# Kernel optimization log

Hardware: AMD Instinct MI355X
Metric: run time of the kernel (lower is better)

Reference implementation:

```python
import jax, jax.numpy as jnp
import numpy as np

HEAD_DIM = 64
SCALE = 1.0 / np.sqrt(HEAD_DIM).astype(np.float32)
EPS = 1e-6


def setup_inputs() -> dict:
    key = jax.random.key(0)
    kq, kk, kv = jax.random.split(key, 3)
    shape = (2, 16, 2048, HEAD_DIM)  # [B, H, S, D]
    return {
        "q": jax.random.normal(kq, shape, dtype=jnp.float32),
        "k": jax.random.normal(kk, shape, dtype=jnp.float32),
        "v": jax.random.normal(kv, shape, dtype=jnp.float32),
    }


def reference(q, k, v):
    # scores: [B, H, S, S]
    scores = jnp.einsum("bhqd,bhkd->bhqk", q, k) * SCALE
    num = scores * scores  # p = 2 power normalization
    den = num.sum(axis=-1, keepdims=True) + EPS
    prob = num / den
    out = jnp.einsum("bhqk,bhkd->bhqd", prob, v)
    return (out, prob)
```

## Files before the change

### kernel.cpp

```cpp
#include <hip/hip_runtime.h>
#include <stdint.h>

#define S_LEN 2048
#define D_DIM 64
#define NBH   32
#define TQ    128
#define KT    64
#define NT    (S_LEN / KT)
#define RC_G  8
#define SCALE_F 0.125f
#define EPS_F   1e-6f
#define SPSTR 40

typedef unsigned short us;
typedef __attribute__((ext_vector_type(8))) short bf8_t;
typedef __attribute__((ext_vector_type(4))) float f4_t;
typedef __attribute__((ext_vector_type(16))) float f16_t;
typedef __attribute__((ext_vector_type(4))) unsigned int u4_t;

#define MFMA16(a,b,c) __builtin_amdgcn_mfma_f32_16x16x32_bf16((a),(b),(c),0,0,0)
#define MFMA32(a,b,c) __builtin_amdgcn_mfma_f32_32x32x16_bf16((a),(b),(c),0,0,0)

__device__ __forceinline__ unsigned int cvtpk(float lo, float hi) {
  unsigned int d;
  asm("v_cvt_pk_bf16_f32 %0, %1, %2" : "=v"(d) : "v"(lo), "v"(hi));
  return d;
}

union u4bf8 { u4_t u; bf8_t b; };

__global__ __launch_bounds__(256) void g_kernel(const float* __restrict__ kp,
                                                float* __restrict__ gpart) {
  __shared__ __align__(16) float sk[64][68];
  const int bh = blockIdx.x >> 3, rc = blockIdx.x & 7;
  const int t = threadIdx.x;
  const int ti = t >> 4, tj = t & 15;
  float acc[4][4];
#pragma unroll
  for (int a = 0; a < 4; ++a)
#pragma unroll
    for (int b = 0; b < 4; ++b) acc[a][b] = 0.f;
  const float* kb = kp + ((size_t)bh * S_LEN + rc * 256) * D_DIM;
  for (int sub = 0; sub < 4; ++sub) {
    __syncthreads();
    {
      const int r = t >> 2, c0 = (t & 3) * 16;
      const float4* p = (const float4*)(kb + (size_t)(sub * 64 + r) * D_DIM + c0);
      float4 x0 = p[0], x1 = p[1], x2 = p[2], x3 = p[3];
      *(float4*)&sk[r][c0]      = x0;
      *(float4*)&sk[r][c0 + 4]  = x1;
      *(float4*)&sk[r][c0 + 8]  = x2;
      *(float4*)&sk[r][c0 + 12] = x3;
    }
    __syncthreads();
#pragma unroll 4
    for (int r = 0; r < 64; ++r) {
      float4 qi = *(const float4*)&sk[r][ti * 4];
      float4 qj = *(const float4*)&sk[r][tj * 4];
      float iv[4] = {qi.x, qi.y, qi.z, qi.w};
      float jv[4] = {qj.x, qj.y, qj.z, qj.w};
#pragma unroll
      for (int a = 0; a < 4; ++a)
#pragma unroll
        for (int b = 0; b < 4; ++b) acc[a][b] += iv[a] * jv[b];
    }
  }
  float* gb = gpart + ((size_t)(rc * NBH + bh) << 12);
#pragma unroll
  for (int a = 0; a < 4; ++a) {
    f4_t vv = {acc[a][0], acc[a][1], acc[a][2], acc[a][3]};
    *(f4_t*)(gb + (ti * 4 + a) * 64 + tj * 4) = vv;
  }
}

__device__ __forceinline__ bf8_t frag_swz(const us* sp, int row, int cb) {
  return *(const bf8_t*)(sp + row * 64 + ((cb ^ (row & 7)) << 3));
}

__global__ __launch_bounds__(512, 4) void attn_main(const float* __restrict__ q,
                                                    const float* __restrict__ k,
                                                    const float* __restrict__ v,
                                                    const float* __restrict__ gpart,
                                                    float* __restrict__ outp,
                                                    float* __restrict__ probp) {
  __shared__ __align__(16) unsigned char smem[53248];
  us* sK  = (us*)smem;
  us* sVt = (us*)(smem + 16384);
  us* sP  = (us*)(smem + 32768);
  float* sInv = (float*)(smem + 32768);
  float* sRed = (float*)smem;

  const int lin = blockIdx.x;
  const int virt = (lin & 7) * 64 + (lin >> 3);
  const int bh = virt >> 4, qb = virt & 15;
  const int q0 = qb * TQ;
  const int t = threadIdx.x, lane = t & 63, w = t >> 6;
  const int l31 = lane & 31, hi = lane >> 5;
  const int wq = w & 3, kh = w >> 2;

  const float* kbh = k + (size_t)bh * S_LEN * D_DIM;
  const float* vbh = v + (size_t)bh * S_LEN * D_DIM;
  const float* qbh = q + (size_t)bh * S_LEN * D_DIM;

  const int kr = t >> 3, kc = t & 7;
  const int vr = (t & 31) * 2, vc = (t >> 5) * 4;

  float4 pk0, pk1, pva, pvb;
  {
    const float4* kp_ = (const float4*)(kbh + (size_t)kr * D_DIM + kc * 8);
    pk0 = kp_[0]; pk1 = kp_[1];
    const float4* vp0 = (const float4*)(vbh + (size_t)vr * D_DIM + vc);
    const float4* vp1 = (const float4*)(vbh + (size_t)(vr + 1) * D_DIM + vc);
    pva = vp0[0]; pvb = vp1[0];
  }

  bf8_t qA[4];
  {
    const float* qrow = qbh + (size_t)(q0 + wq * 32 + l31) * D_DIM;
#pragma unroll
    for (int s = 0; s < 4; ++s) {
      const float4* qp = (const float4*)(qrow + s * 16 + hi * 8);
      float4 a = qp[0], b = qp[1];
      u4bf8 x;
      x.u[0] = cvtpk(a.x * SCALE_F, a.y * SCALE_F);
      x.u[1] = cvtpk(a.z * SCALE_F, a.w * SCALE_F);
      x.u[2] = cvtpk(b.x * SCALE_F, b.y * SCALE_F);
      x.u[3] = cvtpk(b.z * SCALE_F, b.w * SCALE_F);
      qA[s] = x.b;
    }
  }

  {
    const float* gp = gpart + ((size_t)bh << 12) + (size_t)kr * D_DIM + kc * 8;
    const size_t gstride = (size_t)NBH << 12;
    float4 a = {0.f, 0.f, 0.f, 0.f}, b = {0.f, 0.f, 0.f, 0.f};
#pragma unroll
    for (int rc = 0; rc < RC_G; ++rc) {
      const float4* p = (const float4*)(gp + rc * gstride);
      float4 x = p[0], y = p[1];
      a.x += x.x; a.y += x.y; a.z += x.z; a.w += x.w;
      b.x += y.x; b.y += y.y; b.z += y.z; b.w += y.w;
    }
    u4bf8 x;
    x.u[0] = cvtpk(a.x, a.y); x.u[1] = cvtpk(a.z, a.w);
    x.u[2] = cvtpk(b.x, b.y); x.u[3] = cvtpk(b.z, b.w);
    *(u4_t*)(sK + kr * 64 + ((kc ^ (kr & 7)) << 3)) = x.u;
  }
  __syncthreads();

  {
    const int lr = lane & 15, lh = lane >> 4;
    bf8_t qD[2];
    {
      const float* qbase = qbh + (size_t)(q0 + w * 16 + lr) * D_DIM;
#pragma unroll
      for (int h2 = 0; h2 < 2; ++h2) {
        const float4* qp = (const float4*)(qbase + h2 * 32 + lh * 8);
        float4 a = qp[0], b = qp[1];
        u4bf8 x;
        x.u[0] = cvtpk(a.x * SCALE_F, a.y * SCALE_F);
        x.u[1] = cvtpk(a.z * SCALE_F, a.w * SCALE_F);
        x.u[2] = cvtpk(b.x * SCALE_F, b.y * SCALE_F);
        x.u[3] = cvtpk(b.z * SCALE_F, b.w * SCALE_F);
        qD[h2] = x.b;
      }
    }
    float den[4] = {0.f, 0.f, 0.f, 0.f};
#pragma unroll
    for (int ct = 0; ct < 4; ++ct) {
      f4_t accT = {0.f, 0.f, 0.f, 0.f};
      bf8_t b0 = frag_swz(sK, ct * 16 + lr, lh);
      bf8_t b1 = frag_swz(sK, ct * 16 + lr, 4 + lh);
      accT = MFMA16(qD[0], b0, accT);
      accT = MFMA16(qD[1], b1, accT);
#pragma unroll
      for (int i = 0; i < 4; ++i) {
        float qv = qbh[(size_t)(q0 + w * 16 + lh * 4 + i) * D_DIM + ct * 16 + lr] * SCALE_F;
        den[i] += accT[i] * qv;
      }
    }
#pragma unroll
    for (int i = 0; i < 4; ++i) {
      den[i] += __shfl_xor(den[i], 1, 64);
      den[i] += __shfl_xor(den[i], 2, 64);
      den[i] += __shfl_xor(den[i], 4, 64);
      den[i] += __shfl_xor(den[i], 8, 64);
      sInv[w * 16 + lh * 4 + i] = 1.f / (den[i] + EPS_F);
    }
  }
  __syncthreads();

  float invv[16];
#pragma unroll
  for (int r = 0; r < 16; ++r)
    invv[r] = sInv[wq * 32 + (r & 3) + 8 * (r >> 2) + 4 * hi];
  __syncthreads();

  {
    u4bf8 x;
    x.u[0] = cvtpk(pk0.x, pk0.y); x.u[1] = cvtpk(pk0.z, pk0.w);
    x.u[2] = cvtpk(pk1.x, pk1.y); x.u[3] = cvtpk(pk1.z, pk1.w);
    *(u4_t*)(sK + kr * 64 + ((kc ^ (kr & 7)) << 3)) = x.u;
    unsigned int w0 = cvtpk(pva.x, pvb.x), w1 = cvtpk(pva.y, pvb.y);
    unsigned int w2 = cvtpk(pva.z, pvb.z), w3 = cvtpk(pva.w, pvb.w);
    const int cks = vr >> 3, sub = vr & 7;
    *(unsigned int*)(sVt + (vc + 0) * 64 + ((cks ^ ((vc + 0) & 7)) << 3) + sub) = w0;
    *(unsigned int*)(sVt + (vc + 1) * 64 + ((cks ^ ((vc + 1) & 7)) << 3) + sub) = w1;
    *(unsigned int*)(sVt + (vc + 2) * 64 + ((cks ^ ((vc + 2) & 7)) << 3) + sub) = w2;
    *(unsigned int*)(sVt + (vc + 3) * 64 + ((cks ^ ((vc + 3) & 7)) << 3) + sub) = w3;
  }
  __syncthreads();

  f16_t oaccA, oaccB;
#pragma unroll
  for (int i = 0; i < 16; ++i) { oaccA[i] = 0.f; oaccB[i] = 0.f; }

  us* sPw = sP + w * (32 * SPSTR);
  float* probw = probp + ((size_t)bh * S_LEN + q0 + wq * 32) * S_LEN + kh * 32 + l31;

  for (int kt = 0; kt < NT; ++kt) {
    const int cur = kt & 1, nxt = cur ^ 1;
    const us* sKc = sK + cur * 4096;
    const us* sVc = sVt + cur * 4096;
    us* sKn = sK + nxt * 4096;
    us* sVn = sVt + nxt * 4096;
    const int k0 = kt * KT;

    if (kt + 1 < NT) {
      const int k0n = k0 + KT;
      const float4* kp_ = (const float4*)(kbh + (size_t)(k0n + kr) * D_DIM + kc * 8);
      pk0 = kp_[0]; pk1 = kp_[1];
      const float4* vp0 = (const float4*)(vbh + (size_t)(k0n + vr) * D_DIM + vc);
      const float4* vp1 = (const float4*)(vbh + (size_t)(k0n + vr + 1) * D_DIM + vc);
      pva = vp0[0]; pvb = vp1[0];
    }

    f16_t cacc;
#pragma unroll
    for (int i = 0; i < 16; ++i) cacc[i] = 0.f;
#pragma unroll
    for (int s = 0; s < 4; ++s) {
      bf8_t bk = frag_swz(sKc, kh * 32 + l31, 2 * s + hi);
      cacc = MFMA32(qA[s], bk, cacc);
    }

#pragma unroll
    for (int a = 0; a < 4; ++a) {
      float p0 = cacc[4 * a + 0] * cacc[4 * a + 0] * invv[4 * a + 0];
      float p1 = cacc[4 * a + 1] * cacc[4 * a + 1] * invv[4 * a + 1];
      float p2 = cacc[4 * a + 2] * cacc[4 * a + 2] * invv[4 * a + 2];
      float p3 = cacc[4 * a + 3] * cacc[4 * a + 3] * invv[4 * a + 3];
      const int qq = 8 * a + 4 * hi;
      __builtin_nontemporal_store(p0, probw + (size_t)(qq + 0) * S_LEN + k0);
      __builtin_nontemporal_store(p1, probw + (size_t)(qq + 1) * S_LEN + k0);
      __builtin_nontemporal_store(p2, probw + (size_t)(qq + 2) * S_LEN + k0);
      __builtin_nontemporal_store(p3, probw + (size_t)(qq + 3) * S_LEN + k0);
      unsigned int c01 = cvtpk(p0, p1);
      unsigned int c23 = cvtpk(p2, p3);
      sPw[(qq + 0) * SPSTR + l31] = (us)(c01 & 0xffffu);
      sPw[(qq + 1) * SPSTR + l31] = (us)(c01 >> 16);
      sPw[(qq + 2) * SPSTR + l31] = (us)(c23 & 0xffffu);
      sPw[(qq + 3) * SPSTR + l31] = (us)(c23 >> 16);
    }

    bf8_t pa0 = *(const bf8_t*)(sPw + l31 * SPSTR + 0 * 16 + hi * 8);
    bf8_t pa1 = *(const bf8_t*)(sPw + l31 * SPSTR + 1 * 16 + hi * 8);

    bf8_t vb00 = frag_swz(sVc, 0 * 32 + l31, kh * 4 + 2 * 0 + hi);
    bf8_t vb01 = frag_swz(sVc, 1 * 32 + l31, kh * 4 + 2 * 0 + hi);
    bf8_t vb10 = frag_swz(sVc, 0 * 32 + l31, kh * 4 + 2 * 1 + hi);
    bf8_t vb11 = frag_swz(sVc, 1 * 32 + l31, kh * 4 + 2 * 1 + hi);

    oaccA = MFMA32(pa0, vb00, oaccA);
    oaccB = MFMA32(pa0, vb01, oaccB);
    oaccA = MFMA32(pa1, vb10, oaccA);
    oaccB = MFMA32(pa1, vb11, oaccB);

    if (kt + 1 < NT) {
      u4bf8 x;
      x.u[0] = cvtpk(pk0.x, pk0.y); x.u[1] = cvtpk(pk0.z, pk0.w);
      x.u[2] = cvtpk(pk1.x, pk1.y); x.u[3] = cvtpk(pk1.z, pk1.w);
      *(u4_t*)(sKn + kr * 64 + ((kc ^ (kr & 7)) << 3)) = x.u;
      unsigned int w0 = cvtpk(pva.x, pvb.x), w1 = cvtpk(pva.y, pvb.y);
      unsigned int w2 = cvtpk(pva.z, pvb.z), w3 = cvtpk(pva.w, pvb.w);
      const int cks = vr >> 3, sub = vr & 7;
      *(unsigned int*)(sVn + (vc + 0) * 64 + ((cks ^ ((vc + 0) & 7)) << 3) + sub) = w0;
      *(unsigned int*)(sVn + (vc + 1) * 64 + ((cks ^ ((vc + 1) & 7)) << 3) + sub) = w1;
      *(unsigned int*)(sVn + (vc + 2) * 64 + ((cks ^ ((vc + 2) & 7)) << 3) + sub) = w2;
      *(unsigned int*)(sVn + (vc + 3) * 64 + ((cks ^ ((vc + 3) & 7)) << 3) + sub) = w3;
    }
    __syncthreads();
  }

  if (kh == 1) {
    float* dst = sRed + wq * 2048;
#pragma unroll
    for (int i = 0; i < 4; ++i) {
      f4_t ga = {oaccA[4 * i], oaccA[4 * i + 1], oaccA[4 * i + 2], oaccA[4 * i + 3]};
      f4_t gb = {oaccB[4 * i], oaccB[4 * i + 1], oaccB[4 * i + 2], oaccB[4 * i + 3]};
      *(f4_t*)(dst + 0 * 1024 + i * 256 + lane * 4) = ga;
      *(f4_t*)(dst + 1 * 1024 + i * 256 + lane * 4) = gb;
    }
  }
  __syncthreads();
  if (kh == 0) {
    const float* src = sRed + wq * 2048;
    float* ob = outp + ((size_t)bh * S_LEN + q0 + wq * 32) * D_DIM + l31;
#pragma unroll
    for (int i = 0; i < 4; ++i) {
      f4_t ga = *(const f4_t*)(src + 0 * 1024 + i * 256 + lane * 4);
      f4_t gb = *(const f4_t*)(src + 1 * 1024 + i * 256 + lane * 4);
#pragma unroll
      for (int b = 0; b < 4; ++b) {
        const int r = 4 * i + b;
        const int qr = (r & 3) + 8 * (r >> 2) + 4 * hi;
        __builtin_nontemporal_store(oaccA[r] + ga[b], ob + (size_t)qr * D_DIM + 0);
        __builtin_nontemporal_store(oaccB[r] + gb[b], ob + (size_t)qr * D_DIM + 32);
      }
    }
  }
}

extern "C" void kernel_launch(void* const* d_in, const int* in_sizes, int n_in,
                              void* d_out, int out_size, void* d_ws, size_t ws_size,
                              hipStream_t stream) {
  (void)in_sizes; (void)n_in; (void)out_size; (void)ws_size;
  const float* q = (const float*)d_in[0];
  const float* k = (const float*)d_in[1];
  const float* v = (const float*)d_in[2];
  float* outp  = (float*)d_out;
  float* probp = outp + (size_t)NBH * S_LEN * D_DIM;
  float* gpart = (float*)d_ws;

  g_kernel<<<dim3(NBH * RC_G), dim3(256), 0, stream>>>(k, gpart);
  attn_main<<<dim3(512), dim3(512), 0, stream>>>(q, k, v, gpart, outp, probp);
}
```

Baseline: 139.0 us.

## Stage prob tiles in swizzled LDS and write them back as float4 rows

The bf16 P tile for two key tiles is kept in a larger, XOR-swizzled LDS buffer shared by the whole block. Every second iteration, the block reads it back and writes 128-column row segments of prob to global memory with vectorized nontemporal float4 stores. This replaces the per-lane scalar stores and aims for wider, better-coalesced writes of the prob output, which dominates memory traffic. The cost is extra LDS use (64 KB), which may lower occupancy, plus an extra barrier. Prob values are now written from bf16-rounded data, so the output loses precision compared with the fp32 values it stored before.

```diff
diff --git a/kernel.cpp b/kernel.cpp
--- a/kernel.cpp
+++ b/kernel.cpp
@@ -10,7 +10,6 @@
 #define RC_G  8
 #define SCALE_F 0.125f
 #define EPS_F   1e-6f
-#define SPSTR 40
 
 typedef unsigned short us;
 typedef __attribute__((ext_vector_type(8))) short bf8_t;
@@ -83,10 +82,10 @@
                                                     const float* __restrict__ gpart,
                                                     float* __restrict__ outp,
                                                     float* __restrict__ probp) {
-  __shared__ __align__(16) unsigned char smem[53248];
+  __shared__ __align__(16) unsigned char smem[65536];
   us* sK  = (us*)smem;
   us* sVt = (us*)(smem + 16384);
-  us* sP  = (us*)(smem + 32768);
+  unsigned char* Pb = smem + 32768;
   float* sInv = (float*)(smem + 32768);
   float* sRed = (float*)smem;
 
@@ -215,9 +214,6 @@
 #pragma unroll
   for (int i = 0; i < 16; ++i) { oaccA[i] = 0.f; oaccB[i] = 0.f; }
 
-  us* sPw = sP + w * (32 * SPSTR);
-  float* probw = probp + ((size_t)bh * S_LEN + q0 + wq * 32) * S_LEN + kh * 32 + l31;
-
   for (int kt = 0; kt < NT; ++kt) {
     const int cur = kt & 1, nxt = cur ^ 1;
     const us* sKc = sK + cur * 4096;
@@ -244,27 +240,27 @@
       cacc = MFMA32(qA[s], bk, cacc);
     }
 
+    const int cb  = ((kt & 1) << 3) | (kh << 2) | (l31 >> 3);
+    const int inb = (l31 & 7) * 2;
 #pragma unroll
     for (int a = 0; a < 4; ++a) {
       float p0 = cacc[4 * a + 0] * cacc[4 * a + 0] * invv[4 * a + 0];
       float p1 = cacc[4 * a + 1] * cacc[4 * a + 1] * invv[4 * a + 1];
       float p2 = cacc[4 * a + 2] * cacc[4 * a + 2] * invv[4 * a + 2];
       float p3 = cacc[4 * a + 3] * cacc[4 * a + 3] * invv[4 * a + 3];
-      const int qq = 8 * a + 4 * hi;
-      __builtin_nontemporal_store(p0, probw + (size_t)(qq + 0) * S_LEN + k0);
-      __builtin_nontemporal_store(p1, probw + (size_t)(qq + 1) * S_LEN + k0);
-      __builtin_nontemporal_store(p2, probw + (size_t)(qq + 2) * S_LEN + k0);
-      __builtin_nontemporal_store(p3, probw + (size_t)(qq + 3) * S_LEN + k0);
       unsigned int c01 = cvtpk(p0, p1);
       unsigned int c23 = cvtpk(p2, p3);
-      sPw[(qq + 0) * SPSTR + l31] = (us)(c01 & 0xffffu);
-      sPw[(qq + 1) * SPSTR + l31] = (us)(c01 >> 16);
-      sPw[(qq + 2) * SPSTR + l31] = (us)(c23 & 0xffffu);
-      sPw[(qq + 3) * SPSTR + l31] = (us)(c23 >> 16);
-    }
-
-    bf8_t pa0 = *(const bf8_t*)(sPw + l31 * SPSTR + 0 * 16 + hi * 8);
-    bf8_t pa1 = *(const bf8_t*)(sPw + l31 * SPSTR + 1 * 16 + hi * 8);
+      const int r0 = wq * 32 + 8 * a + 4 * hi;
+      *(us*)(Pb + (r0 + 0) * 256 + (((cb ^ ((r0 + 0) & 7))) << 4) + inb) = (us)(c01 & 0xffffu);
+      *(us*)(Pb + (r0 + 1) * 256 + (((cb ^ ((r0 + 1) & 7))) << 4) + inb) = (us)(c01 >> 16);
+      *(us*)(Pb + (r0 + 2) * 256 + (((cb ^ ((r0 + 2) & 7))) << 4) + inb) = (us)(c23 & 0xffffu);
+      *(us*)(Pb + (r0 + 3) * 256 + (((cb ^ ((r0 + 3) & 7))) << 4) + inb) = (us)(c23 >> 16);
+    }
+
+    const int cA = ((kt & 1) << 3) | (kh << 2);
+    const int prow = wq * 32 + l31;
+    bf8_t pa0 = *(const bf8_t*)(Pb + prow * 256 + (((cA + 0 + hi) ^ (prow & 7)) << 4));
+    bf8_t pa1 = *(const bf8_t*)(Pb + prow * 256 + (((cA + 2 + hi) ^ (prow & 7)) << 4));
 
     bf8_t vb00 = frag_swz(sVc, 0 * 32 + l31, kh * 4 + 2 * 0 + hi);
     bf8_t vb01 = frag_swz(sVc, 1 * 32 + l31, kh * 4 + 2 * 0 + hi);
@@ -290,6 +286,25 @@
       *(unsigned int*)(sVn + (vc + 3) * 64 + ((cks ^ ((vc + 3) & 7)) << 3) + sub) = w3;
     }
     __syncthreads();
+
+    if (kt & 1) {
+      float* pbg = probp + ((size_t)bh * S_LEN + q0) * S_LEN + (kt >> 1) * 128 + l31 * 4;
+      const int chL = (l31 >> 1);
+      const int sub8 = (l31 & 1) * 8;
+#pragma unroll
+      for (int i = 0; i < 8; ++i) {
+        const int r = w * 16 + i * 2 + hi;
+        unsigned long long d = *(const unsigned long long*)(Pb + r * 256 + (((chL ^ (r & 7))) << 4) + sub8);
+        unsigned int d0 = (unsigned int)d, d1 = (unsigned int)(d >> 32);
+        f4_t o;
+        o[0] = __uint_as_float(d0 << 16);
+        o[1] = __uint_as_float(d0 & 0xffff0000u);
+        o[2] = __uint_as_float(d1 << 16);
+        o[3] = __uint_as_float(d1 & 0xffff0000u);
+        __builtin_nontemporal_store(o, (f4_t*)(pbg + (size_t)r * S_LEN));
+      }
+      __syncthreads();
+    }
   }
 
   if (kh == 1) {
```

Result: slower. 203.8 us (+46.6%).

## Halve query tile to 64 rows with 256-thread blocks and single-buffered V

Applied to the files above, without the earlier changes.

Shrinks the query tile from 128 to 64 rows, launching twice as many 256-thread blocks, and reassigns K/V staging so each thread loads twice as much. V goes from double-buffered to single-buffered shared memory, with an extra barrier inside the loop before V is overwritten, cutting LDS per block. The aim is more resident blocks and better latency hiding across the 2048x2048 probability writes. In exchange K/V tiles are reloaded twice as often per head and each iteration now has two block-wide barriers.

```diff
diff --git a/kernel.cpp b/kernel.cpp
--- a/kernel.cpp
+++ b/kernel.cpp
@@ -4,7 +4,7 @@
 #define S_LEN 2048
 #define D_DIM 64
 #define NBH   32
-#define TQ    128
+#define TQ    64
 #define KT    64
 #define NT    (S_LEN / KT)
 #define RC_G  8
@@ -77,41 +77,41 @@
   return *(const bf8_t*)(sp + row * 64 + ((cb ^ (row & 7)) << 3));
 }
 
-__global__ __launch_bounds__(512, 4) void attn_main(const float* __restrict__ q,
+__global__ __launch_bounds__(256, 4) void attn_main(const float* __restrict__ q,
                                                     const float* __restrict__ k,
                                                     const float* __restrict__ v,
                                                     const float* __restrict__ gpart,
                                                     float* __restrict__ outp,
                                                     float* __restrict__ probp) {
-  __shared__ __align__(16) unsigned char smem[53248];
+  __shared__ __align__(16) unsigned char smem[34816];
   us* sK  = (us*)smem;
   us* sVt = (us*)(smem + 16384);
-  us* sP  = (us*)(smem + 32768);
-  float* sInv = (float*)(smem + 32768);
+  us* sP  = (us*)(smem + 24576);
+  float* sInv = (float*)(smem + 24576);
   float* sRed = (float*)smem;
 
   const int lin = blockIdx.x;
-  const int virt = (lin & 7) * 64 + (lin >> 3);
-  const int bh = virt >> 4, qb = virt & 15;
+  const int virt = (lin & 7) * 128 + (lin >> 3);
+  const int bh = virt >> 5, qb = virt & 31;
   const int q0 = qb * TQ;
   const int t = threadIdx.x, lane = t & 63, w = t >> 6;
   const int l31 = lane & 31, hi = lane >> 5;
-  const int wq = w & 3, kh = w >> 2;
+  const int wq = w & 1, kh = w >> 1;
 
   const float* kbh = k + (size_t)bh * S_LEN * D_DIM;
   const float* vbh = v + (size_t)bh * S_LEN * D_DIM;
   const float* qbh = q + (size_t)bh * S_LEN * D_DIM;
 
-  const int kr = t >> 3, kc = t & 7;
-  const int vr = (t & 31) * 2, vc = (t >> 5) * 4;
-
-  float4 pk0, pk1, pva, pvb;
-  {
-    const float4* kp_ = (const float4*)(kbh + (size_t)kr * D_DIM + kc * 8);
-    pk0 = kp_[0]; pk1 = kp_[1];
-    const float4* vp0 = (const float4*)(vbh + (size_t)vr * D_DIM + vc);
-    const float4* vp1 = (const float4*)(vbh + (size_t)(vr + 1) * D_DIM + vc);
-    pva = vp0[0]; pvb = vp1[0];
+  const int kr = t >> 2, kc16 = t & 3;
+  const int vr = (t & 31) * 2, vcg = (t >> 5) * 8;
+
+  float4 pk0, pk1, pk2, pk3, pva0, pva1, pvb0, pvb1;
+  {
+    const float4* kp_ = (const float4*)(kbh + (size_t)kr * D_DIM + kc16 * 16);
+    pk0 = kp_[0]; pk1 = kp_[1]; pk2 = kp_[2]; pk3 = kp_[3];
+    const float4* vp0 = (const float4*)(vbh + (size_t)vr * D_DIM + vcg);
+    const float4* vp1 = (const float4*)(vbh + (size_t)(vr + 1) * D_DIM + vcg);
+    pva0 = vp0[0]; pva1 = vp0[1]; pvb0 = vp1[0]; pvb1 = vp1[1];
   }
 
   bf8_t qA[4];
@@ -131,20 +131,26 @@
   }
 
   {
-    const float* gp = gpart + ((size_t)bh << 12) + (size_t)kr * D_DIM + kc * 8;
+    const float* gp = gpart + ((size_t)bh << 12) + (size_t)kr * D_DIM + kc16 * 16;
     const size_t gstride = (size_t)NBH << 12;
-    float4 a = {0.f, 0.f, 0.f, 0.f}, b = {0.f, 0.f, 0.f, 0.f};
+    float4 a0 = {0,0,0,0}, a1 = {0,0,0,0}, a2 = {0,0,0,0}, a3 = {0,0,0,0};
 #pragma unroll
     for (int rc = 0; rc < RC_G; ++rc) {
       const float4* p = (const float4*)(gp + rc * gstride);
-      float4 x = p[0], y = p[1];
-      a.x += x.x; a.y += x.y; a.z += x.z; a.w += x.w;
-      b.x += y.x; b.y += y.y; b.z += y.z; b.w += y.w;
-    }
-    u4bf8 x;
-    x.u[0] = cvtpk(a.x, a.y); x.u[1] = cvtpk(a.z, a.w);
-    x.u[2] = cvtpk(b.x, b.y); x.u[3] = cvtpk(b.z, b.w);
-    *(u4_t*)(sK + kr * 64 + ((kc ^ (kr & 7)) << 3)) = x.u;
+      float4 x0 = p[0], x1 = p[1], x2 = p[2], x3 = p[3];
+      a0.x += x0.x; a0.y += x0.y; a0.z += x0.z; a0.w += x0.w;
+      a1.x += x1.x; a1.y += x1.y; a1.z += x1.z; a1.w += x1.w;
+      a2.x += x2.x; a2.y += x2.y; a2.z += x2.z; a2.w += x2.w;
+      a3.x += x3.x; a3.y += x3.y; a3.z += x3.z; a3.w += x3.w;
+    }
+    u4bf8 x0, x1;
+    x0.u[0] = cvtpk(a0.x, a0.y); x0.u[1] = cvtpk(a0.z, a0.w);
+    x0.u[2] = cvtpk(a1.x, a1.y); x0.u[3] = cvtpk(a1.z, a1.w);
+    x1.u[0] = cvtpk(a2.x, a2.y); x1.u[1] = cvtpk(a2.z, a2.w);
+    x1.u[2] = cvtpk(a3.x, a3.y); x1.u[3] = cvtpk(a3.z, a3.w);
+    const int c0 = 2 * kc16;
+    *(u4_t*)(sK + kr * 64 + (((c0    ) ^ (kr & 7)) << 3)) = x0.u;
+    *(u4_t*)(sK + kr * 64 + (((c0 + 1) ^ (kr & 7)) << 3)) = x1.u;
   }
   __syncthreads();
 
@@ -197,17 +203,23 @@
   __syncthreads();
 
   {
-    u4bf8 x;
-    x.u[0] = cvtpk(pk0.x, pk0.y); x.u[1] = cvtpk(pk0.z, pk0.w);
-    x.u[2] = cvtpk(pk1.x, pk1.y); x.u[3] = cvtpk(pk1.z, pk1.w);
-    *(u4_t*)(sK + kr * 64 + ((kc ^ (kr & 7)) << 3)) = x.u;
-    unsigned int w0 = cvtpk(pva.x, pvb.x), w1 = cvtpk(pva.y, pvb.y);
-    unsigned int w2 = cvtpk(pva.z, pvb.z), w3 = cvtpk(pva.w, pvb.w);
+    u4bf8 x0, x1;
+    x0.u[0] = cvtpk(pk0.x, pk0.y); x0.u[1] = cvtpk(pk0.z, pk0.w);
+    x0.u[2] = cvtpk(pk1.x, pk1.y); x0.u[3] = cvtpk(pk1.z, pk1.w);
+    x1.u[0] = cvtpk(pk2.x, pk2.y); x1.u[1] = cvtpk(pk2.z, pk2.w);
+    x1.u[2] = cvtpk(pk3.x, pk3.y); x1.u[3] = cvtpk(pk3.z, pk3.w);
+    const int c0 = 2 * kc16;
+    *(u4_t*)(sK + kr * 64 + (((c0    ) ^ (kr & 7)) << 3)) = x0.u;
+    *(u4_t*)(sK + kr * 64 + (((c0 + 1) ^ (kr & 7)) << 3)) = x1.u;
+    unsigned int wv[8];
+    wv[0] = cvtpk(pva0.x, pvb0.x); wv[1] = cvtpk(pva0.y, pvb0.y);
+    wv[2] = cvtpk(pva0.z, pvb0.z); wv[3] = cvtpk(pva0.w, pvb0.w);
+    wv[4] = cvtpk(pva1.x, pvb1.x); wv[5] = cvtpk(pva1.y, pvb1.y);
+    wv[6] = cvtpk(pva1.z, pvb1.z); wv[7] = cvtpk(pva1.w, pvb1.w);
     const int cks = vr >> 3, sub = vr & 7;
-    *(unsigned int*)(sVt + (vc + 0) * 64 + ((cks ^ ((vc + 0) & 7)) << 3) + sub) = w0;
-    *(unsigned int*)(sVt + (vc + 1) * 64 + ((cks ^ ((vc + 1) & 7)) << 3) + sub) = w1;
-    *(unsigned int*)(sVt + (vc + 2) * 64 + ((cks ^ ((vc + 2) & 7)) << 3) + sub) = w2;
-    *(unsigned int*)(sVt + (vc + 3) * 64 + ((cks ^ ((vc + 3) & 7)) << 3) + sub) = w3;
+#pragma unroll
+    for (int j = 0; j < 8; ++j)
+      *(unsigned int*)(sVt + (vcg + j) * 64 + ((cks ^ ((vcg + j) & 7)) << 3) + sub) = wv[j];
   }
   __syncthreads();
 
@@ -221,18 +233,12 @@
   for (int kt = 0; kt < NT; ++kt) {
     const int cur = kt & 1, nxt = cur ^ 1;
     const us* sKc = sK + cur * 4096;
-    const us* sVc = sVt + cur * 4096;
     us* sKn = sK + nxt * 4096;
-    us* sVn = sVt + nxt * 4096;
     const int k0 = kt * KT;
 
     if (kt + 1 < NT) {
-      const int k0n = k0 + KT;
-      const float4* kp_ = (const float4*)(kbh + (size_t)(k0n + kr) * D_DIM + kc * 8);
-      pk0 = kp_[0]; pk1 = kp_[1];
-      const float4* vp0 = (const float4*)(vbh + (size_t)(k0n + vr) * D_DIM + vc);
-      const float4* vp1 = (const float4*)(vbh + (size_t)(k0n + vr + 1) * D_DIM + vc);
-      pva = vp0[0]; pvb = vp1[0];
+      const float4* kp_ = (const float4*)(kbh + (size_t)(k0 + KT + kr) * D_DIM + kc16 * 16);
+      pk0 = kp_[0]; pk1 = kp_[1]; pk2 = kp_[2]; pk3 = kp_[3];
     }
 
     f16_t cacc;
@@ -242,6 +248,23 @@
     for (int s = 0; s < 4; ++s) {
       bf8_t bk = frag_swz(sKc, kh * 32 + l31, 2 * s + hi);
       cacc = MFMA32(qA[s], bk, cacc);
+    }
+
+    if (kt + 1 < NT) {
+      u4bf8 x0, x1;
+      x0.u[0] = cvtpk(pk0.x, pk0.y); x0.u[1] = cvtpk(pk0.z, pk0.w);
+      x0.u[2] = cvtpk(pk1.x, pk1.y); x0.u[3] = cvtpk(pk1.z, pk1.w);
+      x1.u[0] = cvtpk(pk2.x, pk2.y); x1.u[1] = cvtpk(pk2.z, pk2.w);
+      x1.u[2] = cvtpk(pk3.x, pk3.y); x1.u[3] = cvtpk(pk3.z, pk3.w);
+      const int c0 = 2 * kc16;
+      *(u4_t*)(sKn + kr * 64 + (((c0    ) ^ (kr & 7)) << 3)) = x0.u;
+      *(u4_t*)(sKn + kr * 64 + (((c0 + 1) ^ (kr & 7)) << 3)) = x1.u;
+    }
+
+    if (kt + 1 < NT) {
+      const float4* vp0 = (const float4*)(vbh + (size_t)(k0 + KT + vr) * D_DIM + vcg);
+      const float4* vp1 = (const float4*)(vbh + (size_t)(k0 + KT + vr + 1) * D_DIM + vcg);
+      pva0 = vp0[0]; pva1 = vp0[1]; pvb0 = vp1[0]; pvb1 = vp1[1];
     }
 
 #pragma unroll
@@ -265,30 +288,30 @@
 
     bf8_t pa0 = *(const bf8_t*)(sPw + l31 * SPSTR + 0 * 16 + hi * 8);
     bf8_t pa1 = *(const bf8_t*)(sPw + l31 * SPSTR + 1 * 16 + hi * 8);
-
-    bf8_t vb00 = frag_swz(sVc, 0 * 32 + l31, kh * 4 + 2 * 0 + hi);
-    bf8_t vb01 = frag_swz(sVc, 1 * 32 + l31, kh * 4 + 2 * 0 + hi);
-    bf8_t vb10 = frag_swz(sVc, 0 * 32 + l31, kh * 4 + 2 * 1 + hi);
-    bf8_t vb11 = frag_swz(sVc, 1 * 32 + l31, kh * 4 + 2 * 1 + hi);
+    bf8_t vb00 = frag_swz(sVt, 0 * 32 + l31, kh * 4 + 2 * 0 + hi);
+    bf8_t vb01 = frag_swz(sVt, 1 * 32 + l31, kh * 4 + 2 * 0 + hi);
+    bf8_t vb10 = frag_swz(sVt, 0 * 32 + l31, kh * 4 + 2 * 1 + hi);
+    bf8_t vb11 = frag_swz(sVt, 1 * 32 + l31, kh * 4 + 2 * 1 + hi);
+
+    __syncthreads();
+
+    if (kt + 1 < NT) {
+      unsigned int wv[8];
+      wv[0] = cvtpk(pva0.x, pvb0.x); wv[1] = cvtpk(pva0.y, pvb0.y);
+      wv[2] = cvtpk(pva0.z, pvb0.z); wv[3] = cvtpk(pva0.w, pvb0.w);
+      wv[4] = cvtpk(pva1.x, pvb1.x); wv[5] = cvtpk(pva1.y, pvb1.y);
+      wv[6] = cvtpk(pva1.z, pvb1.z); wv[7] = cvtpk(pva1.w, pvb1.w);
+      const int cks = vr >> 3, sub = vr & 7;
+#pragma unroll
+      for (int j = 0; j < 8; ++j)
+        *(unsigned int*)(sVt + (vcg + j) * 64 + ((cks ^ ((vcg + j) & 7)) << 3) + sub) = wv[j];
+    }
 
     oaccA = MFMA32(pa0, vb00, oaccA);
     oaccB = MFMA32(pa0, vb01, oaccB);
     oaccA = MFMA32(pa1, vb10, oaccA);
     oaccB = MFMA32(pa1, vb11, oaccB);
 
-    if (kt + 1 < NT) {
-      u4bf8 x;
-      x.u[0] = cvtpk(pk0.x, pk0.y); x.u[1] = cvtpk(pk0.z, pk0.w);
-      x.u[2] = cvtpk(pk1.x, pk1.y); x.u[3] = cvtpk(pk1.z, pk1.w);
-      *(u4_t*)(sKn + kr * 64 + ((kc ^ (kr & 7)) << 3)) = x.u;
-      unsigned int w0 = cvtpk(pva.x, pvb.x), w1 = cvtpk(pva.y, pvb.y);
-      unsigned int w2 = cvtpk(pva.z, pvb.z), w3 = cvtpk(pva.w, pvb.w);
-      const int cks = vr >> 3, sub = vr & 7;
-      *(unsigned int*)(sVn + (vc + 0) * 64 + ((cks ^ ((vc + 0) & 7)) << 3) + sub) = w0;
-      *(unsigned int*)(sVn + (vc + 1) * 64 + ((cks ^ ((vc + 1) & 7)) << 3) + sub) = w1;
-      *(unsigned int*)(sVn + (vc + 2) * 64 + ((cks ^ ((vc + 2) & 7)) << 3) + sub) = w2;
-      *(unsigned int*)(sVn + (vc + 3) * 64 + ((cks ^ ((vc + 3) & 7)) << 3) + sub) = w3;
-    }
     __syncthreads();
   }
 
@@ -333,5 +356,5 @@
   float* gpart = (float*)d_ws;
 
   g_kernel<<<dim3(NBH * RC_G), dim3(256), 0, stream>>>(k, gpart);
-  attn_main<<<dim3(512), dim3(512), 0, stream>>>(q, k, v, gpart, outp, probp);
-}
+  attn_main<<<dim3(NBH * 32), dim3(256), 0, stream>>>(q, k, v, gpart, outp, probp);
+}
```

Measured after the change: 156.7 us. +12.7%, slower.
